# Optimization experiments

Measured on AMD Instinct MI355X. Metric: run time of the kernel, lower is better.

Reference implementation:

```python
import jax, jax.numpy as jnp
import numpy as np

NEG = -9e15

def setup_inputs() -> dict:
    key = jax.random.key(0)
    kH, kA, kW, ka = jax.random.split(key, 4)
    B, N, Din, Dout, Hh = 4, 2048, 128, 32, 8
    H = jax.random.normal(kH, (B, N, Din), dtype=jnp.float32)
    adj = jax.random.randint(kA, (B, N, N), 0, 2, dtype=jnp.int32)
    W = jax.random.normal(kW, (Hh, Din, Dout), dtype=jnp.float32) * (1.0 / np.sqrt(Din))
    a = jax.random.normal(ka, (Hh, 2 * Dout, 1), dtype=jnp.float32) * 0.1
    return {"H": H, "adj": adj, "W": W, "a": a}

def reference(H, adj, W, a):
    # H: [B,N,Din], adj: [B,N,N], W: [h,Din,D], a: [h,2D,1]
    B, N, _ = H.shape
    h, _, D = W.shape
    Wh = jnp.einsum('bni,hio->bhno', H, W)            # [B,h,N,D]
    a1 = a[:, :D, 0]                                   # [h,D] (source/query half)
    a2 = a[:, D:, 0]                                   # [h,D] (neighbor half)
    ei = jnp.einsum('bhnd,hd->bhn', Wh, a1)            # [B,h,N]
    ej = jnp.einsum('bhnd,hd->bhn', Wh, a2)            # [B,h,N]
    e = ei[:, :, :, None] + ej[:, :, None, :]          # [B,h,N,N] == a^T[Wh_i;Wh_j]
    mask = adj[:, None, :, :].astype(bool)             # [B,1,N,N]
    e = jnp.where(mask, e, jnp.float32(NEG))
    alpha = jax.nn.softmax(e, axis=-1)                 # [B,h,N,N]; dropout is identity (eval)
    h_prime = jnp.einsum('bhnm,bhmd->bhnd', alpha, Wh) # [B,h,N,D]
    h_prime = jnp.transpose(h_prime, (0, 2, 1, 3)).reshape(B, N, h * D)
    return jax.nn.relu(h_prime), alpha
```

## Files before the change

kernel.cpp:

```cpp
#include <hip/hip_runtime.h>
#include <stdint.h>

#define BB 4
#define NN 2048
#define DIN 128
#define DOUT 32
#define HH 8
#define NW 64

typedef __bf16 bf16x8 __attribute__((ext_vector_type(8)));
typedef float  f32x4  __attribute__((ext_vector_type(4)));

static __device__ __forceinline__ unsigned short f2b(float f) {
    __bf16 h = (__bf16)f;
    return __builtin_bit_cast(unsigned short, h);
}
static __device__ __forceinline__ float b2f(unsigned short u) {
    union { unsigned int i; float f; } v; v.i = ((unsigned int)u) << 16; return v.f;
}

__global__ __launch_bounds__(256) void k_wht(const float* __restrict__ Hg,
                                             const float* __restrict__ Wg,
                                             unsigned short* __restrict__ WhT)
{
    __shared__ float Hs[DIN * 16];
    const int t  = threadIdx.x;
    const int b  = blockIdx.x >> 7;
    const int n0 = (blockIdx.x & 127) << 4;

    {
        const int r = t >> 4, i0 = (t & 15) << 3;
        const float4* hp = (const float4*)(Hg + ((size_t)(b * NN + n0 + r)) * DIN + i0);
        float4 u0 = hp[0], u1 = hp[1];
        float vv[8] = { u0.x, u0.y, u0.z, u0.w, u1.x, u1.y, u1.z, u1.w };
#pragma unroll
        for (int j = 0; j < 8; j++) Hs[(i0 + j) * 16 + r] = vv[j];
    }
    __syncthreads();

    const int h = t >> 5, d = t & 31;
    f32x4 a0 = {0,0,0,0}, a1 = {0,0,0,0}, a2 = {0,0,0,0}, a3 = {0,0,0,0};
    const float* wp = Wg + h * DIN * DOUT + d;
#pragma unroll 8
    for (int i = 0; i < DIN; i++) {
        float wv = wp[i * DOUT];
        const f32x4* hr = (const f32x4*)&Hs[i * 16];
        a0 += wv * hr[0];
        a1 += wv * hr[1];
        a2 += wv * hr[2];
        a3 += wv * hr[3];
    }
    float v[16] = { a0[0],a0[1],a0[2],a0[3], a1[0],a1[1],a1[2],a1[3],
                    a2[0],a2[1],a2[2],a2[3], a3[0],a3[1],a3[2],a3[3] };
    unsigned int pw[8];
#pragma unroll
    for (int j = 0; j < 8; j++)
        pw[j] = (unsigned int)f2b(v[2*j]) | ((unsigned int)f2b(v[2*j+1]) << 16);
    uint4* dst = (uint4*)(WhT + ((size_t)((b * HH + h) * DOUT + d)) * NN + n0);
    dst[0] = make_uint4(pw[0], pw[1], pw[2], pw[3]);
    dst[1] = make_uint4(pw[4], pw[5], pw[6], pw[7]);
}

__global__ __launch_bounds__(256) void k_bits(const int* __restrict__ adj,
                                              unsigned long long* __restrict__ BM)
{
    size_t tg = (size_t)blockIdx.x * 256 + threadIdx.x;
    unsigned long long m = __ballot(adj[tg] != 0);
    if ((threadIdx.x & 63) == 0) BM[tg >> 6] = m;
}

__global__ __launch_bounds__(256) void k_e(const unsigned short* __restrict__ WhT,
                                           const float* __restrict__ ag,
                                           float* __restrict__ E)
{
    const int blk = blockIdx.x;
    const int bh  = blk >> 3;
    const int h   = bh & 7;
    const int m   = ((blk & 7) << 8) + threadIdx.x;
    const unsigned short* wp = WhT + (size_t)(bh * DOUT) * NN + m;
    float acc = 0.f;
#pragma unroll 8
    for (int dd = 0; dd < DOUT; dd++)
        acc += b2f(wp[(size_t)dd * NN]) * ag[h * 2 * DOUT + DOUT + dd];
    E[(size_t)bh * NN + m] = __expf(acc);
}

__global__ __launch_bounds__(256) void k_main(const float* __restrict__ E,
                                              const unsigned int* __restrict__ BM,
                                              const unsigned short* __restrict__ WhT,
                                              float* __restrict__ out0,
                                              float* __restrict__ out1)
{
    __shared__ float        Es[NN];
    __shared__ unsigned int bits[16][68];
    __shared__ float        red[16][17];
    __shared__ float        invS[16];
    __shared__ __align__(16) __bf16 Ast[4][16][72];
    __shared__ __align__(16) __bf16 Bst[4][32][72];
    __shared__ float        Cred[4][16][33];

    const int t   = threadIdx.x;
    const int bh  = blockIdx.x >> 7;
    const int b   = bh >> 3, h = bh & 7;
    const int n0  = (blockIdx.x & 127) << 4;

    {
        const f32x4* src = (const f32x4*)(E + (size_t)bh * NN);
        f32x4* dst = (f32x4*)Es;
        dst[t]       = src[t];
        dst[t + 256] = src[t + 256];
        const int r = t >> 4, w0 = (t & 15) << 2;
        *(uint4*)&bits[r][w0] =
            *(const uint4*)(BM + ((size_t)(b * NN + n0 + r)) * NW + w0);
    }
    __syncthreads();

    {
        const int r = t >> 4, l = t & 15;
        const unsigned int* br = bits[r];
        float s = 0.f;
#pragma unroll 4
        for (int k2 = 0; k2 < NW; k2++) {
            unsigned int wd = br[k2];
            int m = (k2 << 5) + l;
            if ((wd >> l) & 1)        s += Es[m];
            if ((wd >> (l + 16)) & 1) s += Es[m + 16];
        }
        red[r][l] = s;
    }
    __syncthreads();
    if (t < 16) {
        float s = 0.f;
#pragma unroll
        for (int j = 0; j < 16; j++) s += red[t][j];
        invS[t] = 1.0f / s;
    }
    __syncthreads();

    const int w = t >> 6, lane = t & 63;
    const int r2 = lane >> 2, c4 = lane & 3;
    const int quad = lane >> 4, l16 = lane & 15;
    f32x4 acc[2] = { {0,0,0,0}, {0,0,0,0} };
    const size_t out1row = ((size_t)bh * NN + n0 + r2) * NN;
    const unsigned short* wsrc = WhT + ((size_t)bh * DOUT + (lane >> 1)) * NN
                                     + ((lane & 1) << 5);

    for (int c = 0; c < 8; c++) {
        const int m0 = (w << 9) + (c << 6);
        const int mL = m0 + (c4 << 4);

        {
            const float iv = invS[r2];
            const unsigned int wv =
                (bits[r2][(m0 >> 5) + (c4 >> 1)] >> ((c4 & 1) << 4)) & 0xFFFFu;
            const f32x4* ev = (const f32x4*)&Es[mL];
            float* orow = out1 + out1row + mL;
            unsigned int pk[8];
#pragma unroll
            for (int q = 0; q < 4; q++) {
                f32x4 e4 = ev[q];
                f32x4 x;
                x[0] = ((wv >> (4*q + 0)) & 1) ? e4[0] * iv : 0.f;
                x[1] = ((wv >> (4*q + 1)) & 1) ? e4[1] * iv : 0.f;
                x[2] = ((wv >> (4*q + 2)) & 1) ? e4[2] * iv : 0.f;
                x[3] = ((wv >> (4*q + 3)) & 1) ? e4[3] * iv : 0.f;
                *(f32x4*)(orow + (q << 2)) = x;
                pk[2*q]     = (unsigned int)f2b(x[0]) | ((unsigned int)f2b(x[1]) << 16);
                pk[2*q + 1] = (unsigned int)f2b(x[2]) | ((unsigned int)f2b(x[3]) << 16);
            }
            uint4 q0 = make_uint4(pk[0], pk[1], pk[2], pk[3]);
            uint4 q1 = make_uint4(pk[4], pk[5], pk[6], pk[7]);
            *(bf16x8*)&Ast[w][r2][(c4 << 4)]     = __builtin_bit_cast(bf16x8, q0);
            *(bf16x8*)&Ast[w][r2][(c4 << 4) + 8] = __builtin_bit_cast(bf16x8, q1);
        }

        {
            const uint4* s4 = (const uint4*)(wsrc + m0);
            __bf16* dp = &Bst[w][lane >> 1][(lane & 1) << 5];
#pragma unroll
            for (int k = 0; k < 4; k++)
                *(bf16x8*)(dp + 8*k) = __builtin_bit_cast(bf16x8, s4[k]);
        }

#pragma unroll
        for (int ks = 0; ks < 64; ks += 32) {
            bf16x8 af  = *(const bf16x8*)&Ast[w][l16     ][ks + (quad << 3)];
            bf16x8 bf0 = *(const bf16x8*)&Bst[w][l16     ][ks + (quad << 3)];
            bf16x8 bf1 = *(const bf16x8*)&Bst[w][l16 + 16][ks + (quad << 3)];
            acc[0] = __builtin_amdgcn_mfma_f32_16x16x32_bf16(af, bf0, acc[0], 0, 0, 0);
            acc[1] = __builtin_amdgcn_mfma_f32_16x16x32_bf16(af, bf1, acc[1], 0, 0, 0);
        }
    }

#pragma unroll
    for (int hf = 0; hf < 2; hf++)
#pragma unroll
        for (int i = 0; i < 4; i++)
            Cred[w][(quad << 2) + i][l16 + (hf << 4)] = acc[hf][i];
    __syncthreads();
#pragma unroll
    for (int e = t; e < 512; e += 256) {
        const int r = e >> 5, d = e & 31;
        float v = Cred[0][r][d] + Cred[1][r][d] + Cred[2][r][d] + Cred[3][r][d];
        out0[((size_t)(b * NN + n0 + r)) * (HH * DOUT) + h * DOUT + d] = fmaxf(v, 0.f);
    }
}

extern "C" void kernel_launch(void* const* d_in, const int* in_sizes, int n_in,
                              void* d_out, int out_size, void* d_ws, size_t ws_size,
                              hipStream_t stream)
{
    const float* Hg  = (const float*)d_in[0];
    const int*   adj = (const int*)d_in[1];
    const float* Wg  = (const float*)d_in[2];
    const float* ag  = (const float*)d_in[3];

    float* out0 = (float*)d_out;
    float* out1 = out0 + (size_t)BB * NN * HH * DOUT;

    char* ws = (char*)d_ws;
    unsigned short* WhT = (unsigned short*)ws;
    float*          E   = (float*)(ws + (size_t)BB*HH*DOUT*NN*2);
    unsigned int*   BM  = (unsigned int*)(ws + (size_t)BB*HH*DOUT*NN*2
                                             + (size_t)BB*HH*NN*4);

    k_wht <<<BB * (NN/16),         256, 0, stream>>>(Hg, Wg, WhT);
    k_bits<<<(BB * NN * NN) / 256, 256, 0, stream>>>(adj, (unsigned long long*)BM);
    k_e   <<<BB * HH * (NN/256),   256, 0, stream>>>(WhT, ag, E);
    k_main<<<BB * HH * (NN/16),    256, 0, stream>>>(E, BM, WhT, out0, out1);
}
```

Baseline: 708.8 us.

## Build MFMA operands directly in registers, drop LDS staging, use nontemporal stores

The main loop now has each lane compute its own MFMA A-fragment (the masked, normalized attention values) and load its B-fragment straight from global WhT into registers, matching the 16x16x32 operand layout. This removes the Ast/Bst shared-memory staging and its LDS writes and reads. Alpha and the output are written with nontemporal stores so the large alpha stream does not pollute the cache. In exchange, the alpha stores are narrower per lane (32 bytes at a time, scattered across 16 rows), and each global B load is small.

After: 731.9 us. 1.03x slower.

```diff
diff --git a/kernel.cpp b/kernel.cpp
--- a/kernel.cpp
+++ b/kernel.cpp
@@ -95,8 +95,6 @@
     __shared__ unsigned int bits[16][68];
     __shared__ float        red[16][17];
     __shared__ float        invS[16];
-    __shared__ __align__(16) __bf16 Ast[4][16][72];
-    __shared__ __align__(16) __bf16 Bst[4][32][72];
     __shared__ float        Cred[4][16][33];
 
     const int t   = threadIdx.x;
@@ -138,71 +136,60 @@
     __syncthreads();
 
     const int w = t >> 6, lane = t & 63;
-    const int r2 = lane >> 2, c4 = lane & 3;
-    const int quad = lane >> 4, l16 = lane & 15;
-    f32x4 acc[2] = { {0,0,0,0}, {0,0,0,0} };
-    const size_t out1row = ((size_t)bh * NN + n0 + r2) * NN;
-    const unsigned short* wsrc = WhT + ((size_t)bh * DOUT + (lane >> 1)) * NN
-                                     + ((lane & 1) << 5);
-
-    for (int c = 0; c < 8; c++) {
-        const int m0 = (w << 9) + (c << 6);
-        const int mL = m0 + (c4 << 4);
-
-        {
-            const float iv = invS[r2];
-            const unsigned int wv =
-                (bits[r2][(m0 >> 5) + (c4 >> 1)] >> ((c4 & 1) << 4)) & 0xFFFFu;
-            const f32x4* ev = (const f32x4*)&Es[mL];
-            float* orow = out1 + out1row + mL;
-            unsigned int pk[8];
-#pragma unroll
-            for (int q = 0; q < 4; q++) {
-                f32x4 e4 = ev[q];
-                f32x4 x;
-                x[0] = ((wv >> (4*q + 0)) & 1) ? e4[0] * iv : 0.f;
-                x[1] = ((wv >> (4*q + 1)) & 1) ? e4[1] * iv : 0.f;
-                x[2] = ((wv >> (4*q + 2)) & 1) ? e4[2] * iv : 0.f;
-                x[3] = ((wv >> (4*q + 3)) & 1) ? e4[3] * iv : 0.f;
-                *(f32x4*)(orow + (q << 2)) = x;
-                pk[2*q]     = (unsigned int)f2b(x[0]) | ((unsigned int)f2b(x[1]) << 16);
-                pk[2*q + 1] = (unsigned int)f2b(x[2]) | ((unsigned int)f2b(x[3]) << 16);
-            }
-            uint4 q0 = make_uint4(pk[0], pk[1], pk[2], pk[3]);
-            uint4 q1 = make_uint4(pk[4], pk[5], pk[6], pk[7]);
-            *(bf16x8*)&Ast[w][r2][(c4 << 4)]     = __builtin_bit_cast(bf16x8, q0);
-            *(bf16x8*)&Ast[w][r2][(c4 << 4) + 8] = __builtin_bit_cast(bf16x8, q1);
-        }
-
-        {
-            const uint4* s4 = (const uint4*)(wsrc + m0);
-            __bf16* dp = &Bst[w][lane >> 1][(lane & 1) << 5];
-#pragma unroll
-            for (int k = 0; k < 4; k++)
-                *(bf16x8*)(dp + 8*k) = __builtin_bit_cast(bf16x8, s4[k]);
-        }
-
-#pragma unroll
-        for (int ks = 0; ks < 64; ks += 32) {
-            bf16x8 af  = *(const bf16x8*)&Ast[w][l16     ][ks + (quad << 3)];
-            bf16x8 bf0 = *(const bf16x8*)&Bst[w][l16     ][ks + (quad << 3)];
-            bf16x8 bf1 = *(const bf16x8*)&Bst[w][l16 + 16][ks + (quad << 3)];
-            acc[0] = __builtin_amdgcn_mfma_f32_16x16x32_bf16(af, bf0, acc[0], 0, 0, 0);
-            acc[1] = __builtin_amdgcn_mfma_f32_16x16x32_bf16(af, bf1, acc[1], 0, 0, 0);
-        }
-    }
-
-#pragma unroll
-    for (int hf = 0; hf < 2; hf++)
-#pragma unroll
-        for (int i = 0; i < 4; i++)
-            Cred[w][(quad << 2) + i][l16 + (hf << 4)] = acc[hf][i];
+    const int l16 = lane & 15, quad = lane >> 4;
+    const float iv = invS[l16];
+    float* orow = out1 + ((size_t)bh * NN + n0 + l16) * NN;
+    const unsigned short* brow0 = WhT + ((size_t)bh * DOUT + l16) * NN;
+    const unsigned short* brow1 = brow0 + (size_t)16 * NN;
+    f32x4 acc0 = {0,0,0,0}, acc1 = {0,0,0,0};
+
+#pragma unroll 2
+    for (int c = 0; c < 16; c++) {
+        const int m0 = (w << 9) + (c << 5);
+        const int mb = m0 + (quad << 3);
+
+        bf16x8 b0 = __builtin_bit_cast(bf16x8, *(const uint4*)(brow0 + mb));
+        bf16x8 b1 = __builtin_bit_cast(bf16x8, *(const uint4*)(brow1 + mb));
+
+        const unsigned int wv = (bits[l16][m0 >> 5] >> (quad << 3)) & 0xFFu;
+        f32x4 e0 = *(const f32x4*)&Es[mb];
+        f32x4 e1 = *(const f32x4*)&Es[mb + 4];
+        f32x4 x0, x1;
+        x0[0] = (wv & 0x01) ? e0[0] * iv : 0.f;
+        x0[1] = (wv & 0x02) ? e0[1] * iv : 0.f;
+        x0[2] = (wv & 0x04) ? e0[2] * iv : 0.f;
+        x0[3] = (wv & 0x08) ? e0[3] * iv : 0.f;
+        x1[0] = (wv & 0x10) ? e1[0] * iv : 0.f;
+        x1[1] = (wv & 0x20) ? e1[1] * iv : 0.f;
+        x1[2] = (wv & 0x40) ? e1[2] * iv : 0.f;
+        x1[3] = (wv & 0x80) ? e1[3] * iv : 0.f;
+
+        __builtin_nontemporal_store(x0, (f32x4*)(orow + mb));
+        __builtin_nontemporal_store(x1, (f32x4*)(orow + mb + 4));
+
+        uint4 pk;
+        pk.x = (unsigned int)f2b(x0[0]) | ((unsigned int)f2b(x0[1]) << 16);
+        pk.y = (unsigned int)f2b(x0[2]) | ((unsigned int)f2b(x0[3]) << 16);
+        pk.z = (unsigned int)f2b(x1[0]) | ((unsigned int)f2b(x1[1]) << 16);
+        pk.w = (unsigned int)f2b(x1[2]) | ((unsigned int)f2b(x1[3]) << 16);
+        bf16x8 af = __builtin_bit_cast(bf16x8, pk);
+
+        acc0 = __builtin_amdgcn_mfma_f32_16x16x32_bf16(af, b0, acc0, 0, 0, 0);
+        acc1 = __builtin_amdgcn_mfma_f32_16x16x32_bf16(af, b1, acc1, 0, 0, 0);
+    }
+
+#pragma unroll
+    for (int i = 0; i < 4; i++) {
+        Cred[w][(quad << 2) + i][l16]      = acc0[i];
+        Cred[w][(quad << 2) + i][l16 + 16] = acc1[i];
+    }
     __syncthreads();
 #pragma unroll
     for (int e = t; e < 512; e += 256) {
         const int r = e >> 5, d = e & 31;
         float v = Cred[0][r][d] + Cred[1][r][d] + Cred[2][r][d] + Cred[3][r][d];
-        out0[((size_t)(b * NN + n0 + r)) * (HH * DOUT) + h * DOUT + d] = fmaxf(v, 0.f);
+        __builtin_nontemporal_store(fmaxf(v, 0.f),
+            out0 + ((size_t)(b * NN + n0 + r)) * (HH * DOUT) + h * DOUT + d);
     }
 }
 
```
